# Optimization experiments

Measured on AMD Instinct MI355X. Metric: run time of the kernel, lower is better.

The kernel has to match this reference:

```python
import jax, jax.numpy as jnp
import numpy as np

# Structure matrix S (n_hos*n_types=6, n_structures=8) and internal int_S (unused in forward)
S_MAT = np.array([[1,0,1,0,0,1,0,1],[0,1,0,1,1,0,0,0],[1,1,0,0,0,0,1,0],[0,0,1,1,0,1,0,0],[0,1,1,0,1,0,0,1],[1,0,0,0,1,0,1,0]], dtype=np.float32)
CONTROL_STRENGTH = 10.0  # self.control_strength
PDHG_ITERS = 150         # fixed-iteration batched primal-dual LP solver
BATCH = 32768
N_STRUCT = 8
N_COMBO = 6


def setup_inputs() -> dict:
    key = jax.random.key(0)
    ks = jax.random.split(key, 9)
    X = jax.random.uniform(ks[0], (BATCH, 2, 3), jnp.float32)  # nonnegative bids
    def lin(k, fan_in, fan_out):
        return jax.random.normal(k, (fan_in, fan_out), jnp.float32) * (1.0 / np.sqrt(fan_in))
    W1 = lin(ks[1], 6, 20);  b1 = jnp.zeros((20,), jnp.float32)
    W2 = lin(ks[2], 20, 20); b2 = jnp.zeros((20,), jnp.float32)
    W3 = lin(ks[3], 20, 20); b3 = jnp.zeros((20,), jnp.float32)
    W4 = lin(ks[4], 20, 8);  b4 = jnp.zeros((8,), jnp.float32)
    S = jnp.asarray(S_MAT)
    return {"X": X, "W1": W1, "b1": b1, "W2": W2, "b2": b2, "W3": W3, "b3": b3,
            "W4": W4, "b4": b4, "S": S, "batch_size": BATCH}


def _mlp(Z, W1, b1, W2, b2, W3, b3, W4, b4):
    h = jnp.tanh(Z @ W1 + b1)
    h = jnp.tanh(h @ W2 + b2)
    h = jnp.tanh(h @ W3 + b3)
    return h @ W4 + b4  # [B, 8]


def _batched_lp(S, z, bvec):
    """Solve, per batch row: max 1'x - c*||x - z||_2  s.t. x>=0, S x <= b.
    Equivalent polytope A x <= b' with A=[S; -I], b'=[b; 0]; solved with PDHG.
    z, bvec: [B, 8], [B, 6]."""
    B = z.shape[0]
    A = jnp.concatenate([S, -jnp.eye(N_STRUCT, dtype=S.dtype)], axis=0)  # [14, 8]
    bfull = jnp.concatenate([bvec, jnp.zeros((B, N_STRUCT), bvec.dtype)], axis=1)  # [B, 14]
    L = jnp.linalg.norm(A)  # Frobenius norm upper-bounds spectral norm
    tau = 1.0 / L
    sigma = 1.0 / L

    def prox_g(v):
        # prox of g(x) = -1'x + c||x - z||_2 (w = ones): shift by tau*w then shrink toward z
        u = v + tau
        d = u - z
        n = jnp.linalg.norm(d, axis=-1, keepdims=True)
        scale = jnp.maximum(0.0, 1.0 - tau * CONTROL_STRENGTH / jnp.maximum(n, 1e-12))
        return z + scale * d

    x0 = jnp.maximum(z, 0.0)
    y0 = jnp.zeros((B, N_COMBO + N_STRUCT), z.dtype)

    def step(carry, _):
        x, xbar, y = carry
        y = jnp.maximum(0.0, y + sigma * (xbar @ A.T - bfull))  # dual ascent + proj >= 0
        x_new = prox_g(x - tau * (y @ A))                        # primal prox step
        return (x_new, 2.0 * x_new - x, y), None

    (x, _, _), _ = jax.lax.scan(step, (x0, x0, y0), None, length=PDHG_ITERS)
    return x


def reference(X, W1, b1, W2, b2, W3, b3, W4, b4, S, batch_size):
    B = X.shape[0]
    Z = X.reshape(B, N_COMBO)              # view(-1, n_hos*n_types)
    z = _mlp(Z, W1, b1, W2, b2, W3, b3, W4, b4)  # neural_net_forward -> [B, 8]
    x1 = _batched_lp(S, z, Z)              # linear_program_forward (W = ones)
    return x1
```

## Files before the change

kernel.cpp:

```cpp
#include <hip/hip_runtime.h>
#include <math.h>


#define N_ITERS 150

__device__ __forceinline__ float fast_tanh(float a) {
    float e = __expf(2.0f * a);
    return 1.0f - 2.0f * __builtin_amdgcn_rcpf(e + 1.0f);
}

__global__ void __launch_bounds__(64)
__attribute__((amdgpu_waves_per_eu(1, 1)))
matchnet_kernel(
    const float* __restrict__ X,
    const float* __restrict__ W1, const float* __restrict__ b1,
    const float* __restrict__ W2, const float* __restrict__ b2,
    const float* __restrict__ W3, const float* __restrict__ b3,
    const float* __restrict__ W4, const float* __restrict__ b4,
    float* __restrict__ out, int B)
{
    __shared__ float sW1[120], sW2[400], sW3[400], sW4[160];
    __shared__ float sb1[20], sb2[20], sb3[20], sb4[8];
    for (int i = threadIdx.x; i < 120; i += blockDim.x) sW1[i] = W1[i];
    for (int i = threadIdx.x; i < 400; i += blockDim.x) sW2[i] = W2[i];
    for (int i = threadIdx.x; i < 400; i += blockDim.x) sW3[i] = W3[i];
    for (int i = threadIdx.x; i < 160; i += blockDim.x) sW4[i] = W4[i];
    if (threadIdx.x < 20) {
        sb1[threadIdx.x] = b1[threadIdx.x];
        sb2[threadIdx.x] = b2[threadIdx.x];
        sb3[threadIdx.x] = b3[threadIdx.x];
    }
    if (threadIdx.x < 8) sb4[threadIdx.x] = b4[threadIdx.x];
    __syncthreads();

    int row = blockIdx.x * blockDim.x + threadIdx.x;
    if (row >= B) return;

    float bb0 = X[row * 6 + 0], bb1 = X[row * 6 + 1], bb2 = X[row * 6 + 2];
    float bb3 = X[row * 6 + 3], bb4 = X[row * 6 + 4], bb5 = X[row * 6 + 5];

    float h1[20], h2[20];
    #pragma unroll
    for (int j = 0; j < 20; j++) {
        float acc = sb1[j];
        acc = fmaf(bb0, sW1[0 * 20 + j], acc);
        acc = fmaf(bb1, sW1[1 * 20 + j], acc);
        acc = fmaf(bb2, sW1[2 * 20 + j], acc);
        acc = fmaf(bb3, sW1[3 * 20 + j], acc);
        acc = fmaf(bb4, sW1[4 * 20 + j], acc);
        acc = fmaf(bb5, sW1[5 * 20 + j], acc);
        h1[j] = fast_tanh(acc);
    }
    #pragma unroll
    for (int j = 0; j < 20; j++) {
        float acc = sb2[j];
        #pragma unroll
        for (int i = 0; i < 20; i++) acc = fmaf(h1[i], sW2[i * 20 + j], acc);
        h2[j] = fast_tanh(acc);
    }
    #pragma unroll
    for (int j = 0; j < 20; j++) {
        float acc = sb3[j];
        #pragma unroll
        for (int i = 0; i < 20; i++) acc = fmaf(h2[i], sW3[i * 20 + j], acc);
        h1[j] = fast_tanh(acc);
    }
    float z0, z1, z2, z3, z4, z5, z6, z7;
    {
        float zt[8];
        #pragma unroll
        for (int k = 0; k < 8; k++) {
            float acc = sb4[k];
            #pragma unroll
            for (int i = 0; i < 20; i++) acc = fmaf(h1[i], sW4[i * 8 + k], acc);
            zt[k] = acc;
        }
        z0 = zt[0]; z1 = zt[1]; z2 = zt[2]; z3 = zt[3];
        z4 = zt[4]; z5 = zt[5]; z6 = zt[6]; z7 = zt[7];
    }

    const float tau   = 0.18898223650461363f;
    const float sigma = tau;
    const float tauC  = tau * 10.0f;

    float t0 = tau - z0, t1 = tau - z1, t2 = tau - z2, t3 = tau - z3;
    float t4 = tau - z4, t5 = tau - z5, t6 = tau - z6, t7 = tau - z7;

    float x0 = fmaxf(z0, 0.0f), x1 = fmaxf(z1, 0.0f), x2 = fmaxf(z2, 0.0f), x3 = fmaxf(z3, 0.0f);
    float x4 = fmaxf(z4, 0.0f), x5 = fmaxf(z5, 0.0f), x6 = fmaxf(z6, 0.0f), x7 = fmaxf(z7, 0.0f);
    float xb0 = x0, xb1 = x1, xb2 = x2, xb3 = x3, xb4 = x4, xb5 = x5, xb6 = x6, xb7 = x7;
    float y0 = 0.0f, y1 = 0.0f, y2 = 0.0f, y3 = 0.0f, y4 = 0.0f, y5 = 0.0f;
    float y6 = 0.0f, y7 = 0.0f, y8 = 0.0f, y9 = 0.0f, y10 = 0.0f, y11 = 0.0f, y12 = 0.0f, y13 = 0.0f;

    #pragma unroll 1
    for (int it = 0; it < N_ITERS; it++) {
        float s0 = (xb0 + xb2) + (xb5 + xb7);
        float s1 = (xb1 + xb3) + xb4;
        float s2 = (xb0 + xb1) + xb6;
        float s3 = (xb2 + xb3) + xb5;
        float s4 = (xb1 + xb2) + (xb4 + xb7);
        float s5 = (xb0 + xb4) + xb6;
        y0 = fmaxf(0.0f, fmaf(sigma, s0 - bb0, y0));
        y1 = fmaxf(0.0f, fmaf(sigma, s1 - bb1, y1));
        y2 = fmaxf(0.0f, fmaf(sigma, s2 - bb2, y2));
        y3 = fmaxf(0.0f, fmaf(sigma, s3 - bb3, y3));
        y4 = fmaxf(0.0f, fmaf(sigma, s4 - bb4, y4));
        y5 = fmaxf(0.0f, fmaf(sigma, s5 - bb5, y5));
        y6  = fmaxf(0.0f, fmaf(-sigma, xb0, y6));
        y7  = fmaxf(0.0f, fmaf(-sigma, xb1, y7));
        y8  = fmaxf(0.0f, fmaf(-sigma, xb2, y8));
        y9  = fmaxf(0.0f, fmaf(-sigma, xb3, y9));
        y10 = fmaxf(0.0f, fmaf(-sigma, xb4, y10));
        y11 = fmaxf(0.0f, fmaf(-sigma, xb5, y11));
        y12 = fmaxf(0.0f, fmaf(-sigma, xb6, y12));
        y13 = fmaxf(0.0f, fmaf(-sigma, xb7, y13));

        float w0 = (y0 + y2) + (y5 - y6);
        float w1 = (y1 + y2) + (y4 - y7);
        float w2 = (y0 + y3) + (y4 - y8);
        float w3 = (y1 + y3) - y9;
        float w4 = (y1 + y4) + (y5 - y10);
        float w5 = (y0 + y3) - y11;
        float w6 = (y2 + y5) - y12;
        float w7 = (y0 + y4) - y13;

        float d0 = fmaf(-tau, w0, x0 + t0);
        float d1 = fmaf(-tau, w1, x1 + t1);
        float d2 = fmaf(-tau, w2, x2 + t2);
        float d3 = fmaf(-tau, w3, x3 + t3);
        float d4 = fmaf(-tau, w4, x4 + t4);
        float d5 = fmaf(-tau, w5, x5 + t5);
        float d6 = fmaf(-tau, w6, x6 + t6);
        float d7 = fmaf(-tau, w7, x7 + t7);

        float na = fmaf(d1, d1, d0 * d0);
        float nb = fmaf(d3, d3, d2 * d2);
        float nc = fmaf(d5, d5, d4 * d4);
        float nd = fmaf(d7, d7, d6 * d6);
        float nsq = (na + nb) + (nc + nd);

        float rs = __builtin_amdgcn_rsqf(nsq);
        float scale = fmaxf(0.0f, fmaf(-tauC, rs, 1.0f));

        float xn0 = fmaf(scale, d0, z0);
        float xn1 = fmaf(scale, d1, z1);
        float xn2 = fmaf(scale, d2, z2);
        float xn3 = fmaf(scale, d3, z3);
        float xn4 = fmaf(scale, d4, z4);
        float xn5 = fmaf(scale, d5, z5);
        float xn6 = fmaf(scale, d6, z6);
        float xn7 = fmaf(scale, d7, z7);
        xb0 = fmaf(2.0f, xn0, -x0); x0 = xn0;
        xb1 = fmaf(2.0f, xn1, -x1); x1 = xn1;
        xb2 = fmaf(2.0f, xn2, -x2); x2 = xn2;
        xb3 = fmaf(2.0f, xn3, -x3); x3 = xn3;
        xb4 = fmaf(2.0f, xn4, -x4); x4 = xn4;
        xb5 = fmaf(2.0f, xn5, -x5); x5 = xn5;
        xb6 = fmaf(2.0f, xn6, -x6); x6 = xn6;
        xb7 = fmaf(2.0f, xn7, -x7); x7 = xn7;
    }

    float4* out4 = (float4*)out;
    out4[row * 2 + 0] = make_float4(x0, x1, x2, x3);
    out4[row * 2 + 1] = make_float4(x4, x5, x6, x7);
}

extern "C" void kernel_launch(void* const* d_in, const int* in_sizes, int n_in,
                              void* d_out, int out_size, void* d_ws, size_t ws_size,
                              hipStream_t stream) {
    const float* X  = (const float*)d_in[0];
    const float* W1 = (const float*)d_in[1];
    const float* b1 = (const float*)d_in[2];
    const float* W2 = (const float*)d_in[3];
    const float* b2 = (const float*)d_in[4];
    const float* W3 = (const float*)d_in[5];
    const float* b3 = (const float*)d_in[6];
    const float* W4 = (const float*)d_in[7];
    const float* b4 = (const float*)d_in[8];
    float* out = (float*)d_out;

    int B = in_sizes[0] / 6;
    const int block = 64;
    int grid = (B + block - 1) / block;
    hipLaunchKernelGGL(matchnet_kernel, dim3(grid), dim3(block), 0, stream,
                       X, W1, b1, W2, b2, W3, b3, W4, b4, out, B);
}
```

Before: 116.6 us.

## Rescale PDHG duals by tau and force level-ordered schedule with sched barriers

The dual variables are stored pre-multiplied by tau, so the dual update uses a single constant c = tau*sigma and the primal step no longer multiplies by tau. The row sums now share partial sums across constraints, which shortens the per-iteration dependency chain. Scheduling barriers pin the instructions into explicit dependency levels so the single wave per EU issues them in a tight critical-path order. The risk is that the forced ordering prevents better compiler interleaving, and the rescaling slightly changes floating-point rounding.

Result: no change. 115.4 us (-1.0%).

```diff
diff --git a/kernel.cpp b/kernel.cpp
--- a/kernel.cpp
+++ b/kernel.cpp
@@ -3,6 +3,7 @@
 
 
 #define N_ITERS 150
+#define LEVEL() __builtin_amdgcn_sched_barrier(0)
 
 __device__ __forceinline__ float fast_tanh(float a) {
     float e = __expf(2.0f * a);
@@ -79,77 +80,80 @@
         z4 = zt[4]; z5 = zt[5]; z6 = zt[6]; z7 = zt[7];
     }
 
-    const float tau   = 0.18898223650461363f;
-    const float sigma = tau;
-    const float tauC  = tau * 10.0f;
+    const float tau  = 0.18898223650461363f;
+    const float c    = 0.03571428571428571f;
+    const float tauC = 1.8898223650461363f;
 
     float t0 = tau - z0, t1 = tau - z1, t2 = tau - z2, t3 = tau - z3;
     float t4 = tau - z4, t5 = tau - z5, t6 = tau - z6, t7 = tau - z7;
+    float cb0 = c * bb0, cb1 = c * bb1, cb2 = c * bb2;
+    float cb3 = c * bb3, cb4 = c * bb4, cb5 = c * bb5;
 
     float x0 = fmaxf(z0, 0.0f), x1 = fmaxf(z1, 0.0f), x2 = fmaxf(z2, 0.0f), x3 = fmaxf(z3, 0.0f);
     float x4 = fmaxf(z4, 0.0f), x5 = fmaxf(z5, 0.0f), x6 = fmaxf(z6, 0.0f), x7 = fmaxf(z7, 0.0f);
     float xb0 = x0, xb1 = x1, xb2 = x2, xb3 = x3, xb4 = x4, xb5 = x5, xb6 = x6, xb7 = x7;
-    float y0 = 0.0f, y1 = 0.0f, y2 = 0.0f, y3 = 0.0f, y4 = 0.0f, y5 = 0.0f;
-    float y6 = 0.0f, y7 = 0.0f, y8 = 0.0f, y9 = 0.0f, y10 = 0.0f, y11 = 0.0f, y12 = 0.0f, y13 = 0.0f;
+    float YS0 = 0.0f, YS1 = 0.0f, YS2 = 0.0f, YS3 = 0.0f, YS4 = 0.0f, YS5 = 0.0f;
+    float YI0 = 0.0f, YI1 = 0.0f, YI2 = 0.0f, YI3 = 0.0f;
+    float YI4 = 0.0f, YI5 = 0.0f, YI6 = 0.0f, YI7 = 0.0f;
 
     #pragma unroll 1
     for (int it = 0; it < N_ITERS; it++) {
-        float s0 = (xb0 + xb2) + (xb5 + xb7);
-        float s1 = (xb1 + xb3) + xb4;
-        float s2 = (xb0 + xb1) + xb6;
-        float s3 = (xb2 + xb3) + xb5;
-        float s4 = (xb1 + xb2) + (xb4 + xb7);
-        float s5 = (xb0 + xb4) + xb6;
-        y0 = fmaxf(0.0f, fmaf(sigma, s0 - bb0, y0));
-        y1 = fmaxf(0.0f, fmaf(sigma, s1 - bb1, y1));
-        y2 = fmaxf(0.0f, fmaf(sigma, s2 - bb2, y2));
-        y3 = fmaxf(0.0f, fmaf(sigma, s3 - bb3, y3));
-        y4 = fmaxf(0.0f, fmaf(sigma, s4 - bb4, y4));
-        y5 = fmaxf(0.0f, fmaf(sigma, s5 - bb5, y5));
-        y6  = fmaxf(0.0f, fmaf(-sigma, xb0, y6));
-        y7  = fmaxf(0.0f, fmaf(-sigma, xb1, y7));
-        y8  = fmaxf(0.0f, fmaf(-sigma, xb2, y8));
-        y9  = fmaxf(0.0f, fmaf(-sigma, xb3, y9));
-        y10 = fmaxf(0.0f, fmaf(-sigma, xb4, y10));
-        y11 = fmaxf(0.0f, fmaf(-sigma, xb5, y11));
-        y12 = fmaxf(0.0f, fmaf(-sigma, xb6, y12));
-        y13 = fmaxf(0.0f, fmaf(-sigma, xb7, y13));
-
-        float w0 = (y0 + y2) + (y5 - y6);
-        float w1 = (y1 + y2) + (y4 - y7);
-        float w2 = (y0 + y3) + (y4 - y8);
-        float w3 = (y1 + y3) - y9;
-        float w4 = (y1 + y4) + (y5 - y10);
-        float w5 = (y0 + y3) - y11;
-        float w6 = (y2 + y5) - y12;
-        float w7 = (y0 + y4) - y13;
-
-        float d0 = fmaf(-tau, w0, x0 + t0);
-        float d1 = fmaf(-tau, w1, x1 + t1);
-        float d2 = fmaf(-tau, w2, x2 + t2);
-        float d3 = fmaf(-tau, w3, x3 + t3);
-        float d4 = fmaf(-tau, w4, x4 + t4);
-        float d5 = fmaf(-tau, w5, x5 + t5);
-        float d6 = fmaf(-tau, w6, x6 + t6);
-        float d7 = fmaf(-tau, w7, x7 + t7);
-
-        float na = fmaf(d1, d1, d0 * d0);
-        float nb = fmaf(d3, d3, d2 * d2);
-        float nc = fmaf(d5, d5, d4 * d4);
-        float nd = fmaf(d7, d7, d6 * d6);
-        float nsq = (na + nb) + (nc + nd);
-
+        float p02 = xb0 + xb2, p57 = xb5 + xb7, p13 = xb1 + xb3;
+        float p23 = xb2 + xb3, p12 = xb1 + xb2, p47 = xb4 + xb7;
+        float p06 = xb0 + xb6;
+        float u0 = fmaf(-c, xb0, YI0), u1 = fmaf(-c, xb1, YI1);
+        float u2 = fmaf(-c, xb2, YI2), u3 = fmaf(-c, xb3, YI3);
+        float u4 = fmaf(-c, xb4, YI4), u5 = fmaf(-c, xb5, YI5);
+        float u6 = fmaf(-c, xb6, YI6), u7 = fmaf(-c, xb7, YI7);
+        float e0 = x0 + t0, e1 = x1 + t1, e2 = x2 + t2, e3 = x3 + t3;
+        float e4 = x4 + t4, e5 = x5 + t5, e6 = x6 + t6, e7 = x7 + t7;
+        LEVEL();
+        float s0 = p02 + p57, s1 = p13 + xb4, s2 = p06 + xb1;
+        float s3 = p23 + xb5, s4 = p12 + p47, s5 = p06 + xb4;
+        YI0 = fmaxf(0.0f, u0); YI1 = fmaxf(0.0f, u1);
+        YI2 = fmaxf(0.0f, u2); YI3 = fmaxf(0.0f, u3);
+        YI4 = fmaxf(0.0f, u4); YI5 = fmaxf(0.0f, u5);
+        YI6 = fmaxf(0.0f, u6); YI7 = fmaxf(0.0f, u7);
+        LEVEL();
+        float v0 = fmaf(c, s0, YS0), v1 = fmaf(c, s1, YS1);
+        float v2 = fmaf(c, s2, YS2), v3 = fmaf(c, s3, YS3);
+        float v4 = fmaf(c, s4, YS4), v5 = fmaf(c, s5, YS5);
+        float dA0 = e0 + YI0, dA1 = e1 + YI1, dA2 = e2 + YI2, dA3 = e3 + YI3;
+        float dA4 = e4 + YI4, dA5 = e5 + YI5, dA6 = e6 + YI6, dA7 = e7 + YI7;
+        LEVEL();
+        v0 -= cb0; v1 -= cb1; v2 -= cb2; v3 -= cb3; v4 -= cb4; v5 -= cb5;
+        LEVEL();
+        YS0 = fmaxf(0.0f, v0); YS1 = fmaxf(0.0f, v1); YS2 = fmaxf(0.0f, v2);
+        YS3 = fmaxf(0.0f, v3); YS4 = fmaxf(0.0f, v4); YS5 = fmaxf(0.0f, v5);
+        LEVEL();
+        float r03 = YS0 + YS3, r25 = YS2 + YS5, r14 = YS1 + YS4;
+        float c3 = YS1 + YS3, c7 = YS0 + YS4;
+        LEVEL();
+        float c0 = YS0 + r25, c1 = r14 + YS2, c2 = r03 + YS4, c4 = r14 + YS5;
+        LEVEL();
+        float d0 = dA0 - c0, d1 = dA1 - c1, d2 = dA2 - c2, d3 = dA3 - c3;
+        float d4 = dA4 - c4, d5 = dA5 - r03, d6 = dA6 - r25, d7 = dA7 - c7;
+        LEVEL();
+        float m0 = d0 * d0, m2 = d2 * d2, m4 = d4 * d4, m6 = d6 * d6;
+        LEVEL();
+        float na = fmaf(d1, d1, m0), nb = fmaf(d3, d3, m2);
+        float nc = fmaf(d5, d5, m4), nd = fmaf(d7, d7, m6);
+        LEVEL();
+        float nab = na + nb, ncd = nc + nd;
+        LEVEL();
+        float nsq = nab + ncd;
+        LEVEL();
         float rs = __builtin_amdgcn_rsqf(nsq);
-        float scale = fmaxf(0.0f, fmaf(-tauC, rs, 1.0f));
-
-        float xn0 = fmaf(scale, d0, z0);
-        float xn1 = fmaf(scale, d1, z1);
-        float xn2 = fmaf(scale, d2, z2);
-        float xn3 = fmaf(scale, d3, z3);
-        float xn4 = fmaf(scale, d4, z4);
-        float xn5 = fmaf(scale, d5, z5);
-        float xn6 = fmaf(scale, d6, z6);
-        float xn7 = fmaf(scale, d7, z7);
+        LEVEL();
+        float sc = fmaf(-tauC, rs, 1.0f);
+        LEVEL();
+        float scale = fmaxf(0.0f, sc);
+        LEVEL();
+        float xn0 = fmaf(scale, d0, z0), xn1 = fmaf(scale, d1, z1);
+        float xn2 = fmaf(scale, d2, z2), xn3 = fmaf(scale, d3, z3);
+        float xn4 = fmaf(scale, d4, z4), xn5 = fmaf(scale, d5, z5);
+        float xn6 = fmaf(scale, d6, z6), xn7 = fmaf(scale, d7, z7);
+        LEVEL();
         xb0 = fmaf(2.0f, xn0, -x0); x0 = xn0;
         xb1 = fmaf(2.0f, xn1, -x1); x1 = xn1;
         xb2 = fmaf(2.0f, xn2, -x2); x2 = xn2;
@@ -158,6 +162,7 @@
         xb5 = fmaf(2.0f, xn5, -x5); x5 = xn5;
         xb6 = fmaf(2.0f, xn6, -x6); x6 = xn6;
         xb7 = fmaf(2.0f, xn7, -x7); x7 = xn7;
+        LEVEL();
     }
 
     float4* out4 = (float4*)out;
```
